# Optimization experiments

Hardware: AMD Instinct MI355X
Metric: run time of the kernel (lower is better)

The kernel has to match this reference:

```python
import jax, jax.numpy as jnp
import numpy as np

N_NODES = 50000
N_EDGES = 1600000
IN_FEATS = 512
N_HIDDEN = 128
N_CLASSES = 40


def setup_inputs() -> dict:
    key = jax.random.key(0)
    k1, k2, k3, k4, k5, k6, k7 = jax.random.split(key, 7)
    features = jax.random.normal(k1, (N_NODES, IN_FEATS), dtype=jnp.float32)
    src = jax.random.randint(k2, (N_EDGES,), 0, N_NODES)
    dst = jax.random.randint(k3, (N_EDGES,), 0, N_NODES)
    # Glorot-ish init for weights, zeros for biases (DGL GraphConv defaults)
    W1 = jax.random.normal(k4, (IN_FEATS, N_HIDDEN), dtype=jnp.float32) / np.sqrt(IN_FEATS)
    b1 = jnp.zeros((N_HIDDEN,), dtype=jnp.float32)
    W2 = jax.random.normal(k5, (N_HIDDEN, N_CLASSES), dtype=jnp.float32) / np.sqrt(N_HIDDEN)
    b2 = jnp.zeros((N_CLASSES,), dtype=jnp.float32)
    return {"features": features, "W1": W1, "b1": b1, "W2": W2, "b2": b2,
            "src": src, "dst": dst}


def _norms(src, dst, n_nodes):
    ones = jnp.ones(src.shape[0], dtype=jnp.float32)
    deg_out = jax.ops.segment_sum(ones, src, num_segments=n_nodes)
    deg_in = jax.ops.segment_sum(ones, dst, num_segments=n_nodes)
    # clamp degree >= 1 as DGL does
    norm_src = jax.lax.rsqrt(jnp.maximum(deg_out, 1.0))
    norm_dst = jax.lax.rsqrt(jnp.maximum(deg_in, 1.0))
    return norm_src, norm_dst


def _graph_conv(x, W, b, src, dst, norm_src, norm_dst, n_nodes):
    # DGL GraphConv with norm='both'; in_feats > out_feats so W applied first
    h = x @ W                                   # [N, out]
    h = h * norm_src[:, None]                   # src-side D^{-1/2}
    msgs = h[src]                               # gather [E, out]
    agg = jax.ops.segment_sum(msgs, dst, num_segments=n_nodes)  # scatter-add
    agg = agg * norm_dst[:, None]               # dst-side D^{-1/2}
    return agg + b


def reference(features, W1, b1, W2, b2, src, dst):
    norm_src, norm_dst = _norms(src, dst, N_NODES)
    h = _graph_conv(features, W1, b1, src, dst, norm_src, norm_dst, N_NODES)
    h = jax.nn.relu(h)
    # dropout is identity at inference
    h = _graph_conv(h, W2, b2, src, dst, norm_src, norm_dst, N_NODES)
    return h
```

## Files before the change

### kernel.cpp

```cpp
#include <hip/hip_runtime.h>

#define N_NODES 50000
#define N_EDGES 1600000
#define IN_FEATS 512
#define N_HIDDEN 128
#define N_CLASSES 40
#define NBKT 782
#define NBLK 800
#define EPB 2000
#define NROWPAD 50048

typedef __attribute__((ext_vector_type(8))) short bf16x8;
typedef __attribute__((ext_vector_type(4))) float f32x4;

__device__ __forceinline__ unsigned short f2bf(float f) {
    unsigned u = __float_as_uint(f);
    u = (u + 0x7FFFu + ((u >> 16) & 1u)) >> 16;
    return (unsigned short)u;
}
__device__ __forceinline__ float bf2f(unsigned short h) {
    return __uint_as_float(((unsigned)h) << 16);
}

__global__ __launch_bounds__(256) void p1_hist(
    const int* __restrict__ src, const int* __restrict__ dst,
    int* __restrict__ histD, int* __restrict__ histS) {
    __shared__ int hd[NBKT], hs[NBKT];
    int t = threadIdx.x, b = blockIdx.x;
    for (int i = t; i < NBKT; i += 256) { hd[i] = 0; hs[i] = 0; }
    __syncthreads();
    int e0 = b * EPB;
    for (int i = t; i < EPB; i += 256) {
        atomicAdd(&hd[dst[e0 + i] >> 6], 1);
        atomicAdd(&hs[src[e0 + i] >> 6], 1);
    }
    __syncthreads();
    for (int i = t; i < NBKT; i += 256) {
        histD[b * NBKT + i] = hd[i];
        histS[b * NBKT + i] = hs[i];
    }
}

__global__ __launch_bounds__(256) void p2_local(
    const int* __restrict__ histD, const int* __restrict__ histS,
    int* __restrict__ baseD, int* __restrict__ baseS,
    int* __restrict__ totD, int* __restrict__ totS) {
    int wv = threadIdx.x >> 6, lane = threadIdx.x & 63;
    int w = blockIdx.x * 4 + wv;
    if (w >= NBKT) return;
    int runD = 0, runS = 0;
#pragma unroll
    for (int c = 0; c < 13; c++) {
        int blk = c * 64 + lane;
        int vD = 0, vS = 0;
        if (blk < NBLK) {
            vD = histD[blk * NBKT + w];
            vS = histS[blk * NBKT + w];
        }
        int iD = vD, iS = vS;
#pragma unroll
        for (int off = 1; off < 64; off <<= 1) {
            int tD = __shfl_up(iD, off);
            int tS = __shfl_up(iS, off);
            if (lane >= off) { iD += tD; iS += tS; }
        }
        if (blk < NBLK) {
            baseD[blk * NBKT + w] = runD + iD - vD;
            baseS[blk * NBKT + w] = runS + iS - vS;
        }
        runD += __shfl(iD, 63);
        runS += __shfl(iS, 63);
    }
    if (lane == 0) { totD[w] = runD; totS[w] = runS; }
}

__global__ __launch_bounds__(1024) void p2_small(
    const int* __restrict__ totD, const int* __restrict__ totS,
    int* __restrict__ bucket_base, int* __restrict__ srcb_base,
    int* __restrict__ offsets) {
    __shared__ int part[1024];
    int t = threadIdx.x;
    int v = (t < NBKT) ? totD[t] : 0;
    part[t] = v;
    __syncthreads();
    for (int off = 1; off < 1024; off <<= 1) {
        int x = (t >= off) ? part[t - off] : 0;
        __syncthreads();
        part[t] += x;
        __syncthreads();
    }
    if (t < NBKT) bucket_base[t] = part[t] - v;
    if (t == 0) { bucket_base[NBKT] = N_EDGES; offsets[N_NODES] = N_EDGES; }
    __syncthreads();
    v = (t < NBKT) ? totS[t] : 0;
    part[t] = v;
    __syncthreads();
    for (int off = 1; off < 1024; off <<= 1) {
        int x = (t >= off) ? part[t - off] : 0;
        __syncthreads();
        part[t] += x;
        __syncthreads();
    }
    if (t < NBKT) srcb_base[t] = part[t] - v;
    if (t == 0) srcb_base[NBKT] = N_EDGES;
}

__global__ __launch_bounds__(256) void p3_scatter(
    const int* __restrict__ src, const int* __restrict__ dst,
    const int* __restrict__ baseD, const int* __restrict__ baseS,
    const int* __restrict__ bucket_base, const int* __restrict__ srcb_base,
    unsigned int* __restrict__ edata, unsigned char* __restrict__ srcv) {
    __shared__ int curD[NBKT], curS[NBKT];
    int t = threadIdx.x, b = blockIdx.x;
    for (int i = t; i < NBKT; i += 256) {
        curD[i] = bucket_base[i] + baseD[b * NBKT + i];
        curS[i] = srcb_base[i] + baseS[b * NBKT + i];
    }
    __syncthreads();
    int e0 = b * EPB;
    for (int i = t; i < EPB; i += 256) {
        int s = src[e0 + i], d = dst[e0 + i];
        int slotD = atomicAdd(&curD[d >> 6], 1);
        edata[slotD] = (unsigned)s | ((unsigned)(d & 63) << 16);
        int slotS = atomicAdd(&curS[s >> 6], 1);
        srcv[slotS] = (unsigned char)(s & 63);
    }
}

__global__ __launch_bounds__(256) void p4_count(
    const int* __restrict__ srcb_base, const unsigned char* __restrict__ srcv,
    float* __restrict__ norm_src) {
    __shared__ int cnt[64];
    int t = threadIdx.x, b = blockIdx.x;
    if (t < 64) cnt[t] = 0;
    __syncthreads();
    int s0 = srcb_base[b], s1 = srcb_base[b + 1];
    for (int i = s0 + t; i < s1; i += 256) atomicAdd(&cnt[srcv[i]], 1);
    __syncthreads();
    if (t < 64) {
        int node = b * 64 + t;
        if (node < N_NODES) norm_src[node] = rsqrtf(fmaxf((float)cnt[t], 1.0f));
    }
}

__global__ __launch_bounds__(256) void p4_build(
    const int* __restrict__ bucket_base, const unsigned int* __restrict__ edata,
    int* __restrict__ offsets, float* __restrict__ norm_dst,
    int* __restrict__ sorted_src) {
    __shared__ int cnt[64], cur[64];
    int t = threadIdx.x, b = blockIdx.x;
    if (t < 64) cnt[t] = 0;
    __syncthreads();
    int s0 = bucket_base[b], s1 = bucket_base[b + 1];
    for (int i = s0 + t; i < s1; i += 256)
        atomicAdd(&cnt[(edata[i] >> 16) & 63], 1);
    __syncthreads();
    if (t == 0) {
        int run = 0;
        for (int i = 0; i < 64; i++) { cur[i] = run; run += cnt[i]; }
    }
    __syncthreads();
    if (t < 64) {
        int node = b * 64 + t;
        if (node < N_NODES) {
            offsets[node] = s0 + cur[t];
            norm_dst[node] = rsqrtf(fmaxf((float)cnt[t], 1.0f));
        }
    }
    __syncthreads();
    for (int i = s0 + t; i < s1; i += 256) {
        unsigned e = edata[i];
        int slot = atomicAdd(&cur[(e >> 16) & 63], 1);
        sorted_src[s0 + slot] = (int)(e & 0xFFFFu);
    }
}

__global__ __launch_bounds__(256) void w1cvt_kernel(const float* __restrict__ W1,
                                                    unsigned short* __restrict__ Wth,
                                                    unsigned short* __restrict__ Wtl) {
    int i = blockIdx.x * 256 + threadIdx.x;
    if (i >= IN_FEATS * N_HIDDEN) return;
    int k = i >> 7, c = i & 127;
    float v = W1[i];
    unsigned short h = f2bf(v);
    Wth[c * IN_FEATS + k] = h;
    Wtl[c * IN_FEATS + k] = f2bf(v - bf2f(h));
}

__global__ __launch_bounds__(256) void w2cvt_kernel(const float* __restrict__ W2,
                                                    unsigned short* __restrict__ Wth,
                                                    unsigned short* __restrict__ Wtl) {
    int i = blockIdx.x * 256 + threadIdx.x;
    if (i >= 48 * 128) return;
    int n = i >> 7, k = i & 127;
    float v = (n < N_CLASSES) ? W2[k * N_CLASSES + n] : 0.f;
    unsigned short h = f2bf(v);
    Wth[n * 128 + k] = h;
    Wtl[n * 128 + k] = f2bf(v - bf2f(h));
}

__global__ __launch_bounds__(256) void gemm1_kernel(
    const float* __restrict__ X, const unsigned short* __restrict__ Wth,
    const unsigned short* __restrict__ Wtl,
    const float* __restrict__ norm_src, unsigned short* __restrict__ Hb) {
    __shared__ __align__(16) unsigned short Xh[128][40];
    __shared__ __align__(16) unsigned short Xl[128][40];
    __shared__ __align__(16) unsigned short Wh[128][40];
    __shared__ __align__(16) unsigned short Wl[128][40];
    const int tid = threadIdx.x;
    const int lane = tid & 63;
    const int wave = tid >> 6;
    const int wr = (wave & 1) * 64;
    const int wc = (wave >> 1) * 64;
    const int row0 = blockIdx.x * 128;
    const int m = lane & 15;
    const int q = lane >> 4;

    f32x4 acc[4][4];
#pragma unroll
    for (int i = 0; i < 4; i++)
#pragma unroll
        for (int j = 0; j < 4; j++) acc[i][j] = (f32x4){0.f, 0.f, 0.f, 0.f};

    for (int k0 = 0; k0 < IN_FEATS; k0 += 32) {
#pragma unroll
        for (int l = 0; l < 4; l++) {
            int s = tid + l * 256;
            int r = s >> 3;
            int kq = (s & 7) * 4;
            float4 v = make_float4(0.f, 0.f, 0.f, 0.f);
            int grow = row0 + r;
            if (grow < N_NODES) v = *(const float4*)&X[(size_t)grow * IN_FEATS + k0 + kq];
            unsigned short h0 = f2bf(v.x), h1 = f2bf(v.y), h2 = f2bf(v.z), h3 = f2bf(v.w);
            unsigned short l0 = f2bf(v.x - bf2f(h0)), l1 = f2bf(v.y - bf2f(h1));
            unsigned short l2 = f2bf(v.z - bf2f(h2)), l3 = f2bf(v.w - bf2f(h3));
            uint2 ph = make_uint2((unsigned)h0 | ((unsigned)h1 << 16),
                                  (unsigned)h2 | ((unsigned)h3 << 16));
            uint2 pl = make_uint2((unsigned)l0 | ((unsigned)l1 << 16),
                                  (unsigned)l2 | ((unsigned)l3 << 16));
            *(uint2*)&Xh[r][kq] = ph;
            *(uint2*)&Xl[r][kq] = pl;
        }
#pragma unroll
        for (int l = 0; l < 2; l++) {
            int s = tid + l * 256;
            int c = s >> 2;
            int kq = (s & 3) * 8;
            *(uint4*)&Wh[c][kq] = *(const uint4*)&Wth[(size_t)c * IN_FEATS + k0 + kq];
            *(uint4*)&Wl[c][kq] = *(const uint4*)&Wtl[(size_t)c * IN_FEATS + k0 + kq];
        }
        __syncthreads();

        bf16x8 ah[4], al[4], bh[4], bl[4];
#pragma unroll
        for (int i = 0; i < 4; i++) {
            ah[i] = *(const bf16x8*)&Xh[wr + i * 16 + m][q * 8];
            al[i] = *(const bf16x8*)&Xl[wr + i * 16 + m][q * 8];
            bh[i] = *(const bf16x8*)&Wh[wc + i * 16 + m][q * 8];
            bl[i] = *(const bf16x8*)&Wl[wc + i * 16 + m][q * 8];
        }
#pragma unroll
        for (int i = 0; i < 4; i++)
#pragma unroll
            for (int j = 0; j < 4; j++) {
                acc[i][j] = __builtin_amdgcn_mfma_f32_16x16x32_bf16(ah[i], bh[j], acc[i][j], 0, 0, 0);
                acc[i][j] = __builtin_amdgcn_mfma_f32_16x16x32_bf16(ah[i], bl[j], acc[i][j], 0, 0, 0);
                acc[i][j] = __builtin_amdgcn_mfma_f32_16x16x32_bf16(al[i], bh[j], acc[i][j], 0, 0, 0);
            }
        __syncthreads();
    }
#pragma unroll
    for (int i = 0; i < 4; i++) {
#pragma unroll
        for (int r = 0; r < 4; r++) {
            int grow = row0 + wr + i * 16 + q * 4 + r;
            if (grow < N_NODES) {
                float sc = norm_src[grow];
#pragma unroll
                for (int j = 0; j < 4; j++)
                    Hb[(size_t)grow * N_HIDDEN + wc + j * 16 + m] = f2bf(acc[i][j][r] * sc);
            }
        }
    }
}

#define ADD8(W)                                               \
    acc0 += __uint_as_float((W).x << 16);                     \
    acc1 += __uint_as_float((W).x & 0xffff0000u);             \
    acc2 += __uint_as_float((W).y << 16);                     \
    acc3 += __uint_as_float((W).y & 0xffff0000u);             \
    acc4 += __uint_as_float((W).z << 16);                     \
    acc5 += __uint_as_float((W).z & 0xffff0000u);             \
    acc6 += __uint_as_float((W).w << 16);                     \
    acc7 += __uint_as_float((W).w & 0xffff0000u);

__global__ __launch_bounds__(256) void agg1_kernel(
    const int* __restrict__ offsets, const int* __restrict__ sorted_src,
    const unsigned short* __restrict__ Hb, const float* __restrict__ norm_dst,
    const float* __restrict__ norm_src, const float* __restrict__ b1,
    unsigned short* __restrict__ H1h, unsigned short* __restrict__ H1l) {
    int wid = (blockIdx.x * 256 + threadIdx.x) >> 6;
    int lane = threadIdx.x & 63;
    if (wid >= N_NODES) return;
    int start = offsets[wid], end = offsets[wid + 1];
    int quad = lane >> 4;
    int c8 = (lane & 15) * 8;
    float acc0 = 0.f, acc1 = 0.f, acc2 = 0.f, acc3 = 0.f;
    float acc4 = 0.f, acc5 = 0.f, acc6 = 0.f, acc7 = 0.f;
    int base = start;
    for (; base + 8 <= end; base += 8) {
        int e0 = sorted_src[base + quad];
        int e1 = sorted_src[base + 4 + quad];
        uint4 w0 = *(const uint4*)&Hb[(size_t)e0 * N_HIDDEN + c8];
        uint4 w1 = *(const uint4*)&Hb[(size_t)e1 * N_HIDDEN + c8];
        ADD8(w0);
        ADD8(w1);
    }
    int rem = end - base;
    if (quad < rem) {
        int e = sorted_src[base + quad];
        uint4 w = *(const uint4*)&Hb[(size_t)e * N_HIDDEN + c8];
        ADD8(w);
    }
    if (quad + 4 < rem) {
        int e = sorted_src[base + 4 + quad];
        uint4 w = *(const uint4*)&Hb[(size_t)e * N_HIDDEN + c8];
        ADD8(w);
    }
    acc0 += __shfl_xor(acc0, 16); acc0 += __shfl_xor(acc0, 32);
    acc1 += __shfl_xor(acc1, 16); acc1 += __shfl_xor(acc1, 32);
    acc2 += __shfl_xor(acc2, 16); acc2 += __shfl_xor(acc2, 32);
    acc3 += __shfl_xor(acc3, 16); acc3 += __shfl_xor(acc3, 32);
    acc4 += __shfl_xor(acc4, 16); acc4 += __shfl_xor(acc4, 32);
    acc5 += __shfl_xor(acc5, 16); acc5 += __shfl_xor(acc5, 32);
    acc6 += __shfl_xor(acc6, 16); acc6 += __shfl_xor(acc6, 32);
    acc7 += __shfl_xor(acc7, 16); acc7 += __shfl_xor(acc7, 32);
    if (quad == 0) {
        float nd = norm_dst[wid];
        float ns = norm_src[wid];
        float4 ba = *(const float4*)&b1[c8];
        float4 bb = *(const float4*)&b1[c8 + 4];
        float o[8];
        o[0] = fmaxf(acc0 * nd + ba.x, 0.f) * ns;
        o[1] = fmaxf(acc1 * nd + ba.y, 0.f) * ns;
        o[2] = fmaxf(acc2 * nd + ba.z, 0.f) * ns;
        o[3] = fmaxf(acc3 * nd + ba.w, 0.f) * ns;
        o[4] = fmaxf(acc4 * nd + bb.x, 0.f) * ns;
        o[5] = fmaxf(acc5 * nd + bb.y, 0.f) * ns;
        o[6] = fmaxf(acc6 * nd + bb.z, 0.f) * ns;
        o[7] = fmaxf(acc7 * nd + bb.w, 0.f) * ns;
        unsigned short hh[8], ll[8];
#pragma unroll
        for (int t = 0; t < 8; t++) {
            hh[t] = f2bf(o[t]);
            ll[t] = f2bf(o[t] - bf2f(hh[t]));
        }
        uint4 ph = make_uint4((unsigned)hh[0] | ((unsigned)hh[1] << 16),
                              (unsigned)hh[2] | ((unsigned)hh[3] << 16),
                              (unsigned)hh[4] | ((unsigned)hh[5] << 16),
                              (unsigned)hh[6] | ((unsigned)hh[7] << 16));
        uint4 pl = make_uint4((unsigned)ll[0] | ((unsigned)ll[1] << 16),
                              (unsigned)ll[2] | ((unsigned)ll[3] << 16),
                              (unsigned)ll[4] | ((unsigned)ll[5] << 16),
                              (unsigned)ll[6] | ((unsigned)ll[7] << 16));
        *(uint4*)&H1h[(size_t)wid * N_HIDDEN + c8] = ph;
        *(uint4*)&H1l[(size_t)wid * N_HIDDEN + c8] = pl;
    }
}

__global__ __launch_bounds__(256) void gemm2_kernel(
    const unsigned short* __restrict__ H1h, const unsigned short* __restrict__ H1l,
    const unsigned short* __restrict__ W2th, const unsigned short* __restrict__ W2tl,
    float* __restrict__ H2p) {
    __shared__ __align__(16) unsigned short Bh[48][136];
    __shared__ __align__(16) unsigned short Bl[48][136];
    const int tid = threadIdx.x;
    for (int i = tid; i < 48 * 16; i += 256) {
        int n = i >> 4, kq = (i & 15) * 8;
        *(uint4*)&Bh[n][kq] = *(const uint4*)&W2th[n * 128 + kq];
        *(uint4*)&Bl[n][kq] = *(const uint4*)&W2tl[n * 128 + kq];
    }
    __syncthreads();
    const int lane = tid & 63;
    const int wave = tid >> 6;
    const int m = lane & 15;
    const int q = lane >> 4;
    const int row0 = blockIdx.x * 128 + wave * 32;

    f32x4 acc[2][3];
#pragma unroll
    for (int i = 0; i < 2; i++)
#pragma unroll
        for (int j = 0; j < 3; j++) acc[i][j] = (f32x4){0.f, 0.f, 0.f, 0.f};

#pragma unroll
    for (int kc = 0; kc < 4; kc++) {
        bf16x8 bh[3], bl[3];
#pragma unroll
        for (int j = 0; j < 3; j++) {
            bh[j] = *(const bf16x8*)&Bh[j * 16 + m][kc * 32 + q * 8];
            bl[j] = *(const bf16x8*)&Bl[j * 16 + m][kc * 32 + q * 8];
        }
#pragma unroll
        for (int i = 0; i < 2; i++) {
            size_t ro = (size_t)(row0 + i * 16 + m) * N_HIDDEN + kc * 32 + q * 8;
            bf16x8 ah = *(const bf16x8*)&H1h[ro];
            bf16x8 al = *(const bf16x8*)&H1l[ro];
#pragma unroll
            for (int j = 0; j < 3; j++) {
                acc[i][j] = __builtin_amdgcn_mfma_f32_16x16x32_bf16(ah, bh[j], acc[i][j], 0, 0, 0);
                acc[i][j] = __builtin_amdgcn_mfma_f32_16x16x32_bf16(ah, bl[j], acc[i][j], 0, 0, 0);
                acc[i][j] = __builtin_amdgcn_mfma_f32_16x16x32_bf16(al, bh[j], acc[i][j], 0, 0, 0);
            }
        }
    }
#pragma unroll
    for (int i = 0; i < 2; i++) {
#pragma unroll
        for (int r = 0; r < 4; r++) {
            int row = row0 + i * 16 + q * 4 + r;
            if (row < N_NODES) {
#pragma unroll
                for (int j = 0; j < 3; j++) {
                    int col = j * 16 + m;
                    if (col < N_CLASSES)
                        H2p[(size_t)row * 64 + col] = acc[i][j][r];
                }
            }
        }
    }
}

__global__ __launch_bounds__(256) void agg2_kernel(
    const int* __restrict__ offsets, const int* __restrict__ sorted_src,
    const float* __restrict__ H2p, const float* __restrict__ norm_dst,
    const float* __restrict__ b2, float* __restrict__ OUT) {
    int wid = (blockIdx.x * 256 + threadIdx.x) >> 6;
    int lane = threadIdx.x & 63;
    if (wid >= N_NODES) return;
    int start = offsets[wid], end = offsets[wid + 1];
    int quad = lane >> 4;
    int c4 = (lane & 15) * 4;
    bool active = c4 < N_CLASSES;
    float4 acc = make_float4(0.f, 0.f, 0.f, 0.f);
    int base = start;
    int nfull = (end - start) & ~7;
    for (; base < start + nfull; base += 8) {
        int e0 = sorted_src[base + quad];
        int e1 = sorted_src[base + 4 + quad];
        if (active) {
            float4 v0 = *(const float4*)&H2p[(size_t)e0 * 64 + c4];
            float4 v1 = *(const float4*)&H2p[(size_t)e1 * 64 + c4];
            acc.x += v0.x + v1.x;
            acc.y += v0.y + v1.y;
            acc.z += v0.z + v1.z;
            acc.w += v0.w + v1.w;
        }
    }
    int rem = end - base;
    int n4 = rem & ~3;
    for (int t = 0; t < n4; t += 4) {
        int e = sorted_src[base + t + quad];
        if (active) {
            float4 v = *(const float4*)&H2p[(size_t)e * 64 + c4];
            acc.x += v.x; acc.y += v.y; acc.z += v.z; acc.w += v.w;
        }
    }
    base += n4;
    if (quad < end - base && active) {
        int e = sorted_src[base + quad];
        float4 v = *(const float4*)&H2p[(size_t)e * 64 + c4];
        acc.x += v.x; acc.y += v.y; acc.z += v.z; acc.w += v.w;
    }
    acc.x += __shfl_xor(acc.x, 16); acc.x += __shfl_xor(acc.x, 32);
    acc.y += __shfl_xor(acc.y, 16); acc.y += __shfl_xor(acc.y, 32);
    acc.z += __shfl_xor(acc.z, 16); acc.z += __shfl_xor(acc.z, 32);
    acc.w += __shfl_xor(acc.w, 16); acc.w += __shfl_xor(acc.w, 32);
    if (lane < 10) {
        float nd = norm_dst[wid];
        float4 b = *(const float4*)&b2[lane * 4];
        acc.x = acc.x * nd + b.x;
        acc.y = acc.y * nd + b.y;
        acc.z = acc.z * nd + b.z;
        acc.w = acc.w * nd + b.w;
        *(float4*)&OUT[(size_t)wid * N_CLASSES + lane * 4] = acc;
    }
}

extern "C" void kernel_launch(void* const* d_in, const int* in_sizes, int n_in,
                              void* d_out, int out_size, void* d_ws, size_t ws_size,
                              hipStream_t stream) {
    const float* X   = (const float*)d_in[0];
    const float* W1  = (const float*)d_in[1];
    const float* b1  = (const float*)d_in[2];
    const float* W2  = (const float*)d_in[3];
    const float* b2  = (const float*)d_in[4];
    const int*   src = (const int*)d_in[5];
    const int*   dst = (const int*)d_in[6];
    float* out = (float*)d_out;

    float* norm_src   = (float*)d_ws;
    float* norm_dst   = norm_src + N_NODES;
    int*   offsets    = (int*)(norm_dst + N_NODES);
    int*   bucket_base = offsets + N_NODES + 16;
    int*   srcb_base  = bucket_base + 800;
    unsigned int* edata = (unsigned int*)(srcb_base + 800);
    unsigned char* srcv = (unsigned char*)(edata + N_EDGES);
    int*   sorted_src = (int*)(edata + N_EDGES) + 400000;
    int*   regionA    = sorted_src + N_EDGES;
    int*   histD      = regionA;
    int*   histS      = regionA + 625600;
    int*   baseD      = regionA + 1251200;
    int*   baseS      = regionA + 1876800;
    int*   totD       = regionA + 2502400;
    int*   totS       = regionA + 2503200;
    unsigned short* Hb = (unsigned short*)regionA;
    float* H2p        = (float*)regionA;
    unsigned short* H1h = (unsigned short*)(regionA + 3200000);
    unsigned short* H1l = H1h + (size_t)NROWPAD * N_HIDDEN;
    unsigned short* W1th = H1l + (size_t)NROWPAD * N_HIDDEN;
    unsigned short* W1tl = W1th + IN_FEATS * N_HIDDEN;
    unsigned short* W2th = W1tl + IN_FEATS * N_HIDDEN;
    unsigned short* W2tl = W2th + 48 * 128;

    p1_hist<<<NBLK, 256, 0, stream>>>(src, dst, histD, histS);
    p2_local<<<(NBKT + 3) / 4, 256, 0, stream>>>(histD, histS, baseD, baseS, totD, totS);
    p2_small<<<1, 1024, 0, stream>>>(totD, totS, bucket_base, srcb_base, offsets);
    p3_scatter<<<NBLK, 256, 0, stream>>>(src, dst, baseD, baseS, bucket_base, srcb_base,
                                         edata, srcv);
    p4_count<<<NBKT, 256, 0, stream>>>(srcb_base, srcv, norm_src);
    p4_build<<<NBKT, 256, 0, stream>>>(bucket_base, edata, offsets, norm_dst, sorted_src);

    w1cvt_kernel<<<(IN_FEATS * N_HIDDEN + 255) / 256, 256, 0, stream>>>(W1, W1th, W1tl);
    w2cvt_kernel<<<(48 * 128 + 255) / 256, 256, 0, stream>>>(W2, W2th, W2tl);
    gemm1_kernel<<<(N_NODES + 127) / 128, 256, 0, stream>>>(X, W1th, W1tl, norm_src, Hb);
    agg1_kernel<<<(N_NODES + 3) / 4, 256, 0, stream>>>(offsets, sorted_src, Hb, norm_dst,
                                                       norm_src, b1, H1h, H1l);
    gemm2_kernel<<<(N_NODES + 127) / 128, 256, 0, stream>>>(H1h, H1l, W2th, W2tl, H2p);
    agg2_kernel<<<(N_NODES + 3) / 4, 256, 0, stream>>>(offsets, sorted_src, H2p, norm_dst, b2, out);
}
```

Before: 409.1 us.

## Restructure gemm1: 64-row tiles, W1 read directly from chunked global layout, prefetch X

The W1 split-bf16 conversion now writes a k-chunked layout so each wave can load its B fragments straight from global or L2 instead of staging them in shared memory. gemm1 switches to 64-row blocks where each wave owns 32 output columns, which roughly doubles the block count. The next X chunk is register-prefetched while the current one is computed, and the bf16 packing uses the paired conversion intrinsic. The cost is that W1 fragments are re-read from cache by every block, and each block gets less reuse per tile.

```diff
diff --git a/kernel.cpp b/kernel.cpp
--- a/kernel.cpp
+++ b/kernel.cpp
@@ -1,4 +1,5 @@
 #include <hip/hip_runtime.h>
+#include <hip/hip_bf16.h>
 
 #define N_NODES 50000
 #define N_EDGES 1600000
@@ -20,6 +21,12 @@
 }
 __device__ __forceinline__ float bf2f(unsigned short h) {
     return __uint_as_float(((unsigned)h) << 16);
+}
+__device__ __forceinline__ unsigned pk_bf(float a, float b) {
+    __hip_bfloat162 h = __float22bfloat162_rn(make_float2(a, b));
+    union { __hip_bfloat162 v; unsigned u; } c;
+    c.v = h;
+    return c.u;
 }
 
 __global__ __launch_bounds__(256) void p1_hist(
@@ -176,15 +183,16 @@
 }
 
 __global__ __launch_bounds__(256) void w1cvt_kernel(const float* __restrict__ W1,
-                                                    unsigned short* __restrict__ Wth,
-                                                    unsigned short* __restrict__ Wtl) {
+                                                    unsigned short* __restrict__ Wch,
+                                                    unsigned short* __restrict__ Wcl) {
     int i = blockIdx.x * 256 + threadIdx.x;
     if (i >= IN_FEATS * N_HIDDEN) return;
     int k = i >> 7, c = i & 127;
     float v = W1[i];
     unsigned short h = f2bf(v);
-    Wth[c * IN_FEATS + k] = h;
-    Wtl[c * IN_FEATS + k] = f2bf(v - bf2f(h));
+    int o = (k >> 5) * 4096 + c * 32 + (k & 31);
+    Wch[o] = h;
+    Wcl[o] = f2bf(v - bf2f(h));
 }
 
 __global__ __launch_bounds__(256) void w2cvt_kernel(const float* __restrict__ W2,
@@ -200,69 +208,73 @@
 }
 
 __global__ __launch_bounds__(256) void gemm1_kernel(
-    const float* __restrict__ X, const unsigned short* __restrict__ Wth,
-    const unsigned short* __restrict__ Wtl,
+    const float* __restrict__ X, const unsigned short* __restrict__ Wch,
+    const unsigned short* __restrict__ Wcl,
     const float* __restrict__ norm_src, unsigned short* __restrict__ Hb) {
-    __shared__ __align__(16) unsigned short Xh[128][40];
-    __shared__ __align__(16) unsigned short Xl[128][40];
-    __shared__ __align__(16) unsigned short Wh[128][40];
-    __shared__ __align__(16) unsigned short Wl[128][40];
+    __shared__ __align__(16) unsigned short Xh[64][40];
+    __shared__ __align__(16) unsigned short Xl[64][40];
     const int tid = threadIdx.x;
     const int lane = tid & 63;
-    const int wave = tid >> 6;
-    const int wr = (wave & 1) * 64;
-    const int wc = (wave >> 1) * 64;
-    const int row0 = blockIdx.x * 128;
+    const int wv = tid >> 6;
     const int m = lane & 15;
     const int q = lane >> 4;
-
-    f32x4 acc[4][4];
+    const int row0 = blockIdx.x * 64;
+
+    const int r0 = tid >> 3,          kq0 = (tid & 7) * 4;
+    const int r1 = (tid + 256) >> 3,  kq1 = (tid & 7) * 4;
+    const bool g0 = (row0 + r0) < N_NODES;
+    const bool g1 = (row0 + r1) < N_NODES;
+    const float* xp0 = &X[(size_t)(row0 + r0) * IN_FEATS + kq0];
+    const float* xp1 = &X[(size_t)(row0 + r1) * IN_FEATS + kq1];
+
+    f32x4 acc[4][2];
 #pragma unroll
     for (int i = 0; i < 4; i++)
 #pragma unroll
-        for (int j = 0; j < 4; j++) acc[i][j] = (f32x4){0.f, 0.f, 0.f, 0.f};
-
-    for (int k0 = 0; k0 < IN_FEATS; k0 += 32) {
-#pragma unroll
-        for (int l = 0; l < 4; l++) {
-            int s = tid + l * 256;
-            int r = s >> 3;
-            int kq = (s & 7) * 4;
-            float4 v = make_float4(0.f, 0.f, 0.f, 0.f);
-            int grow = row0 + r;
-            if (grow < N_NODES) v = *(const float4*)&X[(size_t)grow * IN_FEATS + k0 + kq];
-            unsigned short h0 = f2bf(v.x), h1 = f2bf(v.y), h2 = f2bf(v.z), h3 = f2bf(v.w);
-            unsigned short l0 = f2bf(v.x - bf2f(h0)), l1 = f2bf(v.y - bf2f(h1));
-            unsigned short l2 = f2bf(v.z - bf2f(h2)), l3 = f2bf(v.w - bf2f(h3));
-            uint2 ph = make_uint2((unsigned)h0 | ((unsigned)h1 << 16),
-                                  (unsigned)h2 | ((unsigned)h3 << 16));
-            uint2 pl = make_uint2((unsigned)l0 | ((unsigned)l1 << 16),
-                                  (unsigned)l2 | ((unsigned)l3 << 16));
-            *(uint2*)&Xh[r][kq] = ph;
-            *(uint2*)&Xl[r][kq] = pl;
-        }
-#pragma unroll
-        for (int l = 0; l < 2; l++) {
-            int s = tid + l * 256;
-            int c = s >> 2;
-            int kq = (s & 3) * 8;
-            *(uint4*)&Wh[c][kq] = *(const uint4*)&Wth[(size_t)c * IN_FEATS + k0 + kq];
-            *(uint4*)&Wl[c][kq] = *(const uint4*)&Wtl[(size_t)c * IN_FEATS + k0 + kq];
+        for (int j = 0; j < 2; j++) acc[i][j] = (f32x4){0.f, 0.f, 0.f, 0.f};
+
+    float4 xa0 = g0 ? *(const float4*)xp0 : make_float4(0.f, 0.f, 0.f, 0.f);
+    float4 xa1 = g1 ? *(const float4*)xp1 : make_float4(0.f, 0.f, 0.f, 0.f);
+
+    for (int kc = 0; kc < 16; kc++) {
+        {
+            unsigned h0 = pk_bf(xa0.x, xa0.y), h1 = pk_bf(xa0.z, xa0.w);
+            unsigned l0 = pk_bf(xa0.x - __uint_as_float(h0 << 16),
+                                xa0.y - __uint_as_float(h0 & 0xffff0000u));
+            unsigned l1 = pk_bf(xa0.z - __uint_as_float(h1 << 16),
+                                xa0.w - __uint_as_float(h1 & 0xffff0000u));
+            *(uint2*)&Xh[r0][kq0] = make_uint2(h0, h1);
+            *(uint2*)&Xl[r0][kq0] = make_uint2(l0, l1);
+            unsigned h2 = pk_bf(xa1.x, xa1.y), h3 = pk_bf(xa1.z, xa1.w);
+            unsigned l2 = pk_bf(xa1.x - __uint_as_float(h2 << 16),
+                                xa1.y - __uint_as_float(h2 & 0xffff0000u));
+            unsigned l3 = pk_bf(xa1.z - __uint_as_float(h3 << 16),
+                                xa1.w - __uint_as_float(h3 & 0xffff0000u));
+            *(uint2*)&Xh[r1][kq1] = make_uint2(h2, h3);
+            *(uint2*)&Xl[r1][kq1] = make_uint2(l2, l3);
         }
         __syncthreads();
-
-        bf16x8 ah[4], al[4], bh[4], bl[4];
+        if (kc < 15) {
+            xa0 = g0 ? *(const float4*)(xp0 + (kc + 1) * 32) : make_float4(0.f, 0.f, 0.f, 0.f);
+            xa1 = g1 ? *(const float4*)(xp1 + (kc + 1) * 32) : make_float4(0.f, 0.f, 0.f, 0.f);
+        }
+        bf16x8 bh[2], bl[2];
+#pragma unroll
+        for (int j = 0; j < 2; j++) {
+            int o = kc * 4096 + (wv * 32 + j * 16 + m) * 32 + q * 8;
+            bh[j] = *(const bf16x8*)&Wch[o];
+            bl[j] = *(const bf16x8*)&Wcl[o];
+        }
+        bf16x8 ah[4], al[4];
 #pragma unroll
         for (int i = 0; i < 4; i++) {
-            ah[i] = *(const bf16x8*)&Xh[wr + i * 16 + m][q * 8];
-            al[i] = *(const bf16x8*)&Xl[wr + i * 16 + m][q * 8];
-            bh[i] = *(const bf16x8*)&Wh[wc + i * 16 + m][q * 8];
-            bl[i] = *(const bf16x8*)&Wl[wc + i * 16 + m][q * 8];
+            ah[i] = *(const bf16x8*)&Xh[i * 16 + m][q * 8];
+            al[i] = *(const bf16x8*)&Xl[i * 16 + m][q * 8];
         }
 #pragma unroll
         for (int i = 0; i < 4; i++)
 #pragma unroll
-            for (int j = 0; j < 4; j++) {
+            for (int j = 0; j < 2; j++) {
                 acc[i][j] = __builtin_amdgcn_mfma_f32_16x16x32_bf16(ah[i], bh[j], acc[i][j], 0, 0, 0);
                 acc[i][j] = __builtin_amdgcn_mfma_f32_16x16x32_bf16(ah[i], bl[j], acc[i][j], 0, 0, 0);
                 acc[i][j] = __builtin_amdgcn_mfma_f32_16x16x32_bf16(al[i], bh[j], acc[i][j], 0, 0, 0);
@@ -273,12 +285,12 @@
     for (int i = 0; i < 4; i++) {
 #pragma unroll
         for (int r = 0; r < 4; r++) {
-            int grow = row0 + wr + i * 16 + q * 4 + r;
+            int grow = row0 + i * 16 + q * 4 + r;
             if (grow < N_NODES) {
                 float sc = norm_src[grow];
 #pragma unroll
-                for (int j = 0; j < 4; j++)
-                    Hb[(size_t)grow * N_HIDDEN + wc + j * 16 + m] = f2bf(acc[i][j][r] * sc);
+                for (int j = 0; j < 2; j++)
+                    Hb[(size_t)grow * N_HIDDEN + wv * 32 + j * 16 + m] = f2bf(acc[i][j][r] * sc);
             }
         }
     }
@@ -518,9 +530,9 @@
     float* H2p        = (float*)regionA;
     unsigned short* H1h = (unsigned short*)(regionA + 3200000);
     unsigned short* H1l = H1h + (size_t)NROWPAD * N_HIDDEN;
-    unsigned short* W1th = H1l + (size_t)NROWPAD * N_HIDDEN;
-    unsigned short* W1tl = W1th + IN_FEATS * N_HIDDEN;
-    unsigned short* W2th = W1tl + IN_FEATS * N_HIDDEN;
+    unsigned short* W1ch = H1l + (size_t)NROWPAD * N_HIDDEN;
+    unsigned short* W1cl = W1ch + IN_FEATS * N_HIDDEN;
+    unsigned short* W2th = W1cl + IN_FEATS * N_HIDDEN;
     unsigned short* W2tl = W2th + 48 * 128;
 
     p1_hist<<<NBLK, 256, 0, stream>>>(src, dst, histD, histS);
@@ -531,9 +543,9 @@
     p4_count<<<NBKT, 256, 0, stream>>>(srcb_base, srcv, norm_src);
     p4_build<<<NBKT, 256, 0, stream>>>(bucket_base, edata, offsets, norm_dst, sorted_src);
 
-    w1cvt_kernel<<<(IN_FEATS * N_HIDDEN + 255) / 256, 256, 0, stream>>>(W1, W1th, W1tl);
+    w1cvt_kernel<<<(IN_FEATS * N_HIDDEN + 255) / 256, 256, 0, stream>>>(W1, W1ch, W1cl);
     w2cvt_kernel<<<(48 * 128 + 255) / 256, 256, 0, stream>>>(W2, W2th, W2tl);
-    gemm1_kernel<<<(N_NODES + 127) / 128, 256, 0, stream>>>(X, W1th, W1tl, norm_src, Hb);
+    gemm1_kernel<<<NBKT, 256, 0, stream>>>(X, W1ch, W1cl, norm_src, Hb);
     agg1_kernel<<<(N_NODES + 3) / 4, 256, 0, stream>>>(offsets, sorted_src, Hb, norm_dst,
                                                        norm_src, b1, H1h, H1l);
     gemm2_kernel<<<(N_NODES + 127) / 128, 256, 0, stream>>>(H1h, H1l, W2th, W2tl, H2p);
```

After: 383.9 us. 1.07x faster.
